# Performance work log

Measured on AMD Instinct MI355X. Metric: run time of the kernel, lower is better.

## Reference

```python
import jax, jax.numpy as jnp
import numpy as np

K = 10          # top-k history news selected per candidate
THRESHOLD = 0.1 # attention-weight threshold (config.threshold)
EPS = 1e-12     # F.normalize eps


def setup_inputs() -> dict:
    key = jax.random.key(0)
    k1, k2, k3, k4 = jax.random.split(key, 4)
    B, C, H, L, LEV, D = 32, 5, 50, 32, 3, 256
    return {
        "cdd_repr": jax.random.normal(k1, (B, C, D), dtype=jnp.float32),
        "his_repr": jax.random.normal(k2, (B, H, D), dtype=jnp.float32),
        "his_embedding": jax.random.normal(k3, (B, H, L, LEV, D), dtype=jnp.float32),
        "W_sel": jax.random.normal(k4, (D, D), dtype=jnp.float32) * (1.0 / np.sqrt(D)),
        "b_sel": jnp.zeros((D,), dtype=jnp.float32),
    }


def _l2norm(x):
    # F.normalize(x, dim=-1): x / max(||x||, eps)
    n = jnp.sqrt(jnp.sum(x * x, axis=-1, keepdims=True))
    return x / jnp.maximum(n, EPS)


def reference(cdd_repr, his_repr, his_embedding, W_sel, b_sel):
    # selectionProject (Linear) + L2 normalize
    c = _l2norm(cdd_repr @ W_sel + b_sel)      # [B, C, D]
    h = _l2norm(his_repr @ W_sel + b_sel)      # [B, H, D]
    # news-level attention scores: cdd x his
    attn = jnp.einsum('bcd,bhd->bch', c, h)    # [B, C, H]
    # top-k over history
    w, idx = jax.lax.top_k(attn, K)            # [B, C, K]
    # gather selected history embeddings: [B, C, K, L, LEV, D]
    B = his_embedding.shape[0]
    his_activated = his_embedding[jnp.arange(B)[:, None, None], idx]
    # threshold masking then scale activated embeddings by attention weight
    w_masked = jnp.where(w < THRESHOLD, 0.0, w)
    his_activated = his_activated * w_masked[:, :, :, None, None, None]
    return his_activated
```

## Files before the change

### kernel.cpp

```cpp
#include <hip/hip_runtime.h>
#include <math.h>

#define BB 32
#define CC 5
#define HH 50
#define LL 32
#define LEV 3
#define DD 256
#define KK 10
#define THRESH 0.1f
#define EPSF 1e-12f

__global__ void proj_norm_kernel(const float* __restrict__ cdd,
                                 const float* __restrict__ his,
                                 const float* __restrict__ W,
                                 const float* __restrict__ bias,
                                 float* __restrict__ c_out,
                                 float* __restrict__ h_out)
{
    const int row = blockIdx.x;
    const int j   = threadIdx.x;

    const float* x;
    float* y;
    if (row < BB * CC) {
        x = cdd + (size_t)row * DD;
        y = c_out + (size_t)row * DD;
    } else {
        const int r = row - BB * CC;
        x = his + (size_t)r * DD;
        y = h_out + (size_t)r * DD;
    }

    __shared__ float xs[DD];
    xs[j] = x[j];
    __syncthreads();

    float a0 = 0.f, a1 = 0.f, a2 = 0.f, a3 = 0.f;
    #pragma unroll 4
    for (int d = 0; d < DD; d += 4) {
        a0 += xs[d + 0] * W[(size_t)(d + 0) * DD + j];
        a1 += xs[d + 1] * W[(size_t)(d + 1) * DD + j];
        a2 += xs[d + 2] * W[(size_t)(d + 2) * DD + j];
        a3 += xs[d + 3] * W[(size_t)(d + 3) * DD + j];
    }
    float acc = bias[j] + ((a0 + a1) + (a2 + a3));

    __shared__ float red[DD];
    red[j] = acc * acc;
    __syncthreads();
    for (int s = DD / 2; s > 0; s >>= 1) {
        if (j < s) red[j] += red[j + s];
        __syncthreads();
    }
    const float norm = sqrtf(red[0]);
    const float inv  = 1.0f / fmaxf(norm, EPSF);
    y[j] = acc * inv;
}

__global__ void attn_topk_kernel(const float* __restrict__ c_n,
                                 const float* __restrict__ h_n,
                                 float* __restrict__ w_out,
                                 int* __restrict__ idx_out)
{
    const int bc   = blockIdx.x;
    const int b    = bc / CC;
    const int tid  = threadIdx.x;
    const int wid  = tid >> 6;
    const int lane = tid & 63;

    __shared__ float cs[DD];
    __shared__ float attn_s[HH];
    cs[tid] = c_n[(size_t)bc * DD + tid];
    __syncthreads();

    for (int h = wid; h < HH; h += 4) {
        const float* hr = h_n + (size_t)(b * HH + h) * DD;
        float p = 0.f;
        #pragma unroll
        for (int i = 0; i < 4; ++i) {
            const int d = lane + i * 64;
            p += cs[d] * hr[d];
        }
        #pragma unroll
        for (int off = 32; off > 0; off >>= 1)
            p += __shfl_down(p, off, 64);
        if (lane == 0) attn_s[h] = p;
    }
    __syncthreads();

    if (tid == 0) {
        unsigned long long usedm = 0ull;
        for (int k = 0; k < KK; ++k) {
            float best = -INFINITY;
            int bi = 0;
            for (int h = 0; h < HH; ++h) {
                if (!((usedm >> h) & 1ull) && attn_s[h] > best) {
                    best = attn_s[h];
                    bi = h;
                }
            }
            usedm |= (1ull << bi);
            w_out[bc * KK + k]   = (best < THRESH) ? 0.0f : best;
            idx_out[bc * KK + k] = bi;
        }
    }
}

__global__ void gather_scale_kernel(const float* __restrict__ emb,
                                    const float* __restrict__ w,
                                    const int* __restrict__ idx,
                                    float* __restrict__ out)
{
    const int INNER  = LL * LEV * DD;
    const int INNER4 = INNER / 4;
    const int blk = blockIdx.x;
    const int b   = blk / (CC * KK);

    const float wv = w[blk];
    const int hi   = idx[blk];

    float4* dst = (float4*)(out + (size_t)blk * INNER);

    if (wv == 0.0f) {
        const float4 z = make_float4(0.f, 0.f, 0.f, 0.f);
        for (int i = threadIdx.x; i < INNER4; i += blockDim.x)
            dst[i] = z;
    } else {
        const float4* src = (const float4*)(emb + ((size_t)(b * HH + hi)) * INNER);
        for (int i = threadIdx.x; i < INNER4; i += blockDim.x) {
            float4 v = src[i];
            dst[i] = make_float4(v.x * wv, v.y * wv, v.z * wv, v.w * wv);
        }
    }
}

extern "C" void kernel_launch(void* const* d_in, const int* in_sizes, int n_in,
                              void* d_out, int out_size, void* d_ws, size_t ws_size,
                              hipStream_t stream) {
    const float* cdd  = (const float*)d_in[0];
    const float* his  = (const float*)d_in[1];
    const float* emb  = (const float*)d_in[2];
    const float* W    = (const float*)d_in[3];
    const float* bias = (const float*)d_in[4];
    float* out = (float*)d_out;

    char* ws = (char*)d_ws;
    float* c_n  = (float*)ws;
    float* h_n  = (float*)(ws + 163840);
    float* wv   = (float*)(ws + 163840 + 1638400);
    int*   idx  = (int*)  (ws + 163840 + 1638400 + 6400);

    proj_norm_kernel<<<BB * CC + BB * HH, DD, 0, stream>>>(cdd, his, W, bias, c_n, h_n);
    attn_topk_kernel<<<BB * CC, DD, 0, stream>>>(c_n, h_n, wv, idx);
    gather_scale_kernel<<<BB * CC * KK, 256, 0, stream>>>(emb, wv, idx, out);
}
```

Before: 87.24 us.

## Batch projection rows per block, wave-parallel top-k, chunked nontemporal gather

The projection kernel now handles 8 rows per block, so each W load is reused across rows, and it replaces the shared-memory tree reduction with wave shuffles. Top-k now runs as a wave-wide shuffle argmax repeated K times instead of a serial loop on a single thread. The gather kernel splits each output slice into 4 chunks to launch more blocks, and it uses nontemporal stores for the large output write. Together these cut serial latency in the small kernels and aim to push the memory-bound gather closer to full bandwidth, at the cost of more register use in the projection kernel.

```diff
diff --git a/kernel.cpp b/kernel.cpp
--- a/kernel.cpp
+++ b/kernel.cpp
@@ -10,6 +10,10 @@
 #define KK 10
 #define THRESH 0.1f
 #define EPSF 1e-12f
+#define RPB 8
+#define NROWS (BB * CC + BB * HH)
+
+typedef float f32x4 __attribute__((ext_vector_type(4)));
 
 __global__ void proj_norm_kernel(const float* __restrict__ cdd,
                                  const float* __restrict__ his,
@@ -18,44 +22,61 @@
                                  float* __restrict__ c_out,
                                  float* __restrict__ h_out)
 {
-    const int row = blockIdx.x;
-    const int j   = threadIdx.x;
+    const int row0 = blockIdx.x * RPB;
+    const int j    = threadIdx.x;
+    const int wid  = j >> 6;
+    const int lane = j & 63;
 
-    const float* x;
-    float* y;
-    if (row < BB * CC) {
-        x = cdd + (size_t)row * DD;
-        y = c_out + (size_t)row * DD;
-    } else {
-        const int r = row - BB * CC;
-        x = his + (size_t)r * DD;
-        y = h_out + (size_t)r * DD;
+    __shared__ float xs[RPB][DD];
+    #pragma unroll
+    for (int r = 0; r < RPB; ++r) {
+        const int row = row0 + r;
+        const float* x = (row < BB * CC) ? (cdd + (size_t)row * DD)
+                                         : (his + (size_t)(row - BB * CC) * DD);
+        xs[r][j] = x[j];
+    }
+    __syncthreads();
+
+    const float bj = bias[j];
+    float acc[RPB];
+    #pragma unroll
+    for (int r = 0; r < RPB; ++r) acc[r] = bj;
+
+    for (int d = 0; d < DD; d += 4) {
+        const float w0 = W[(size_t)(d + 0) * DD + j];
+        const float w1 = W[(size_t)(d + 1) * DD + j];
+        const float w2 = W[(size_t)(d + 2) * DD + j];
+        const float w3 = W[(size_t)(d + 3) * DD + j];
+        #pragma unroll
+        for (int r = 0; r < RPB; ++r) {
+            const float4 xv = *(const float4*)&xs[r][d];
+            acc[r] = fmaf(xv.x, w0, fmaf(xv.y, w1, fmaf(xv.z, w2, fmaf(xv.w, w3, acc[r]))));
+        }
     }
 
-    __shared__ float xs[DD];
-    xs[j] = x[j];
+    __shared__ float part[RPB][4];
+    #pragma unroll
+    for (int r = 0; r < RPB; ++r) {
+        float s = acc[r] * acc[r];
+        #pragma unroll
+        for (int off = 32; off > 0; off >>= 1) s += __shfl_xor(s, off, 64);
+        if (lane == 0) part[r][wid] = s;
+    }
+    __syncthreads();
+    __shared__ float inv_s[RPB];
+    if (j < RPB) {
+        const float s = part[j][0] + part[j][1] + part[j][2] + part[j][3];
+        inv_s[j] = 1.0f / fmaxf(sqrtf(s), EPSF);
+    }
     __syncthreads();
 
-    float a0 = 0.f, a1 = 0.f, a2 = 0.f, a3 = 0.f;
-    #pragma unroll 4
-    for (int d = 0; d < DD; d += 4) {
-        a0 += xs[d + 0] * W[(size_t)(d + 0) * DD + j];
-        a1 += xs[d + 1] * W[(size_t)(d + 1) * DD + j];
-        a2 += xs[d + 2] * W[(size_t)(d + 2) * DD + j];
-        a3 += xs[d + 3] * W[(size_t)(d + 3) * DD + j];
+    #pragma unroll
+    for (int r = 0; r < RPB; ++r) {
+        const int row = row0 + r;
+        float* y = (row < BB * CC) ? (c_out + (size_t)row * DD)
+                                   : (h_out + (size_t)(row - BB * CC) * DD);
+        y[j] = acc[r] * inv_s[r];
     }
-    float acc = bias[j] + ((a0 + a1) + (a2 + a3));
-
-    __shared__ float red[DD];
-    red[j] = acc * acc;
-    __syncthreads();
-    for (int s = DD / 2; s > 0; s >>= 1) {
-        if (j < s) red[j] += red[j + s];
-        __syncthreads();
-    }
-    const float norm = sqrtf(red[0]);
-    const float inv  = 1.0f / fmaxf(norm, EPSF);
-    y[j] = acc * inv;
 }
 
 __global__ void attn_topk_kernel(const float* __restrict__ c_n,
@@ -70,43 +91,44 @@
     const int lane = tid & 63;
 
     __shared__ float cs[DD];
-    __shared__ float attn_s[HH];
+    __shared__ float attn_s[64];
     cs[tid] = c_n[(size_t)bc * DD + tid];
+    if (tid < 64) attn_s[tid] = -INFINITY;
     __syncthreads();
 
     for (int h = wid; h < HH; h += 4) {
         const float* hr = h_n + (size_t)(b * HH + h) * DD;
         float p = 0.f;
         #pragma unroll
-        for (int i = 0; i < 4; ++i) {
-            const int d = lane + i * 64;
-            p += cs[d] * hr[d];
-        }
+        for (int i = 0; i < 4; ++i) p += cs[lane + i * 64] * hr[lane + i * 64];
         #pragma unroll
-        for (int off = 32; off > 0; off >>= 1)
-            p += __shfl_down(p, off, 64);
+        for (int off = 32; off > 0; off >>= 1) p += __shfl_down(p, off, 64);
         if (lane == 0) attn_s[h] = p;
     }
     __syncthreads();
 
-    if (tid == 0) {
-        unsigned long long usedm = 0ull;
+    if (wid == 0) {
+        float v   = attn_s[lane];
+        int   myi = lane;
         for (int k = 0; k < KK; ++k) {
-            float best = -INFINITY;
-            int bi = 0;
-            for (int h = 0; h < HH; ++h) {
-                if (!((usedm >> h) & 1ull) && attn_s[h] > best) {
-                    best = attn_s[h];
-                    bi = h;
-                }
+            float bv = v;
+            int   bi = myi;
+            #pragma unroll
+            for (int off = 32; off > 0; off >>= 1) {
+                const float ov = __shfl_xor(bv, off, 64);
+                const int   oi = __shfl_xor(bi, off, 64);
+                if (ov > bv || (ov == bv && oi < bi)) { bv = ov; bi = oi; }
             }
-            usedm |= (1ull << bi);
-            w_out[bc * KK + k]   = (best < THRESH) ? 0.0f : best;
-            idx_out[bc * KK + k] = bi;
+            if (lane == 0) {
+                w_out[bc * KK + k]   = (bv < THRESH) ? 0.0f : bv;
+                idx_out[bc * KK + k] = bi;
+            }
+            if (myi == bi) v = -INFINITY;
         }
     }
 }
 
+#define CHUNKS 4
 __global__ void gather_scale_kernel(const float* __restrict__ emb,
                                     const float* __restrict__ w,
                                     const int* __restrict__ idx,
@@ -114,23 +136,28 @@
 {
     const int INNER  = LL * LEV * DD;
     const int INNER4 = INNER / 4;
-    const int blk = blockIdx.x;
-    const int b   = blk / (CC * KK);
+    const int PER    = INNER4 / CHUNKS;
+
+    const int g     = blockIdx.x;
+    const int blk   = g / CHUNKS;
+    const int chunk = g % CHUNKS;
+    const int b     = blk / (CC * KK);
 
     const float wv = w[blk];
-    const int hi   = idx[blk];
+    const int   hi = idx[blk];
 
-    float4* dst = (float4*)(out + (size_t)blk * INNER);
+    f32x4* dst = (f32x4*)(out + (size_t)blk * INNER) + (size_t)chunk * PER;
 
     if (wv == 0.0f) {
-        const float4 z = make_float4(0.f, 0.f, 0.f, 0.f);
-        for (int i = threadIdx.x; i < INNER4; i += blockDim.x)
-            dst[i] = z;
+        const f32x4 z = (f32x4){0.f, 0.f, 0.f, 0.f};
+        for (int i = threadIdx.x; i < PER; i += 256)
+            __builtin_nontemporal_store(z, &dst[i]);
     } else {
-        const float4* src = (const float4*)(emb + ((size_t)(b * HH + hi)) * INNER);
-        for (int i = threadIdx.x; i < INNER4; i += blockDim.x) {
-            float4 v = src[i];
-            dst[i] = make_float4(v.x * wv, v.y * wv, v.z * wv, v.w * wv);
+        const f32x4* src = (const f32x4*)(emb + (size_t)(b * HH + hi) * INNER)
+                           + (size_t)chunk * PER;
+        for (int i = threadIdx.x; i < PER; i += 256) {
+            const f32x4 v = src[i];
+            __builtin_nontemporal_store(v * wv, &dst[i]);
         }
     }
 }
@@ -146,12 +173,12 @@
     float* out = (float*)d_out;
 
     char* ws = (char*)d_ws;
-    float* c_n  = (float*)ws;
-    float* h_n  = (float*)(ws + 163840);
-    float* wv   = (float*)(ws + 163840 + 1638400);
-    int*   idx  = (int*)  (ws + 163840 + 1638400 + 6400);
+    float* c_n = (float*)ws;
+    float* h_n = (float*)(ws + 163840);
+    float* wv  = (float*)(ws + 163840 + 1638400);
+    int*   idx = (int*)  (ws + 163840 + 1638400 + 6400);
 
-    proj_norm_kernel<<<BB * CC + BB * HH, DD, 0, stream>>>(cdd, his, W, bias, c_n, h_n);
+    proj_norm_kernel<<<NROWS / RPB, DD, 0, stream>>>(cdd, his, W, bias, c_n, h_n);
     attn_topk_kernel<<<BB * CC, DD, 0, stream>>>(c_n, h_n, wv, idx);
-    gather_scale_kernel<<<BB * CC * KK, 256, 0, stream>>>(emb, wv, idx, out);
+    gather_scale_kernel<<<BB * CC * KK * CHUNKS, 256, 0, stream>>>(emb, wv, idx, out);
 }
```

New measurement: 78.29 us. 10.3% less time.
